# Kernel optimization log

Measured on AMD Instinct MI355X. Metric: run time of the kernel, lower is better.

Reference implementation:

```python
import jax, jax.numpy as jnp
import numpy as np

D_MODEL, N_HEADS, D_LLM = 1024, 16, 4096
D_KEYS = D_MODEL // N_HEADS  # 64


def setup_inputs() -> dict:
    key = jax.random.key(0)
    ks = jax.random.split(key, 11)
    s = lambda fan_in: 1.0 / np.sqrt(fan_in)
    inp = {
        "target_embedding": jax.random.normal(ks[0], (4, 2048, D_MODEL), jnp.float32),
        "source_embedding": jax.random.normal(ks[1], (4, 1024, D_LLM), jnp.float32),
        "value_embedding": jax.random.normal(ks[2], (4, 1024, D_LLM), jnp.float32),
        "Wq": jax.random.uniform(ks[3], (D_MODEL, D_KEYS * N_HEADS), jnp.float32, -s(D_MODEL), s(D_MODEL)),
        "bq": jax.random.uniform(ks[4], (D_KEYS * N_HEADS,), jnp.float32, -s(D_MODEL), s(D_MODEL)),
        "Wk": jax.random.uniform(ks[5], (D_LLM, D_KEYS * N_HEADS), jnp.float32, -s(D_LLM), s(D_LLM)),
        "bk": jax.random.uniform(ks[6], (D_KEYS * N_HEADS,), jnp.float32, -s(D_LLM), s(D_LLM)),
        "Wv": jax.random.uniform(ks[7], (D_LLM, D_KEYS * N_HEADS), jnp.float32, -s(D_LLM), s(D_LLM)),
        "bv": jax.random.uniform(ks[8], (D_KEYS * N_HEADS,), jnp.float32, -s(D_LLM), s(D_LLM)),
        "Wo": jax.random.uniform(ks[9], (D_KEYS * N_HEADS, D_MODEL), jnp.float32, -s(D_KEYS * N_HEADS), s(D_KEYS * N_HEADS)),
        "bo": jax.random.uniform(ks[10], (D_MODEL,), jnp.float32, -s(D_KEYS * N_HEADS), s(D_KEYS * N_HEADS)),
    }
    return inp


def reference(target_embedding, source_embedding, value_embedding,
              Wq, bq, Wk, bk, Wv, bv, Wo, bo):
    B, L, _ = target_embedding.shape
    _, S, _ = source_embedding.shape
    H, E = N_HEADS, D_KEYS
    q = (target_embedding @ Wq + bq).reshape(B, L, H, E)
    k = (source_embedding @ Wk + bk).reshape(B, S, H, E)
    v = (value_embedding @ Wv + bv).reshape(B, S, H, E)
    scale = 1.0 / np.sqrt(E)
    scores = jnp.einsum('blhe,bshe->bhls', q, k)  # [B,H,L,S]
    A = jax.nn.softmax(scale * scores, axis=-1)   # dropout = identity (eval mode)
    out = jnp.einsum('bhls,bshe->blhe', A, v).reshape(B, L, H * E)
    return out @ Wo + bo
```

## Files before the change

kernel.cpp:

```cpp
#include <hip/hip_runtime.h>
#include <hip/hip_bf16.h>

using bf16 = __hip_bfloat16;
typedef __attribute__((ext_vector_type(8))) short short8;
typedef __attribute__((ext_vector_type(4))) float f32x4;

static constexpr int Bc = 4, Lc = 2048, Sc = 1024;
static constexpr int DModel = 1024;

__device__ __forceinline__ void gload16(const void* g, void* l) {
  __builtin_amdgcn_global_load_lds((const __attribute__((address_space(1))) void*)g,
                                   (__attribute__((address_space(3))) void*)l,
                                   16, 0, 0);
}

__device__ __forceinline__ void wait_vm8()  { asm volatile("s_waitcnt vmcnt(8)" ::: "memory"); }
__device__ __forceinline__ void wait_vm6()  { asm volatile("s_waitcnt vmcnt(6)" ::: "memory"); }
__device__ __forceinline__ void wait_vm3()  { asm volatile("s_waitcnt vmcnt(3)" ::: "memory"); }
__device__ __forceinline__ void wait_vm2()  { asm volatile("s_waitcnt vmcnt(2)" ::: "memory"); }
__device__ __forceinline__ void wait_vm0()  { asm volatile("s_waitcnt vmcnt(0)" ::: "memory"); }
__device__ __forceinline__ void barrier_raw() { asm volatile("s_barrier" ::: "memory"); }

__global__ __launch_bounds__(256) void prep(
    const float* __restrict__ Wq, bf16* __restrict__ WqT,
    const float* __restrict__ Wk, bf16* __restrict__ WkT,
    const float* __restrict__ Wv, bf16* __restrict__ WvT,
    const float* __restrict__ Wo, bf16* __restrict__ WoT,
    const float* __restrict__ a, bf16* __restrict__ ao, long na4,
    const float* __restrict__ b, bf16* __restrict__ bo, long nb4,
    const float* __restrict__ c, bf16* __restrict__ co, long nc4) {
  __shared__ bf16 tile[32][33];
  int bid = blockIdx.x;
  if (bid < 10240) {
    const float* in; bf16* out; int R, l;
    if (bid < 1024)      { in = Wq; out = WqT; R = 1024; l = bid; }
    else if (bid < 5120) { in = Wk; out = WkT; R = 4096; l = bid - 1024; }
    else if (bid < 9216) { in = Wv; out = WvT; R = 4096; l = bid - 5120; }
    else                 { in = Wo; out = WoT; R = 1024; l = bid - 9216; }
    const int C = 1024;
    int bx = l & 31, by = l >> 5;
    int tx = threadIdx.x & 31, ty = threadIdx.x >> 5;
    int r0 = by * 32, c0 = bx * 32;
#pragma unroll
    for (int i = 0; i < 32; i += 8)
      tile[ty + i][tx] = __float2bfloat16(in[(long)(r0 + ty + i) * C + c0 + tx]);
    __syncthreads();
#pragma unroll
    for (int i = 0; i < 32; i += 8)
      out[(long)(c0 + ty + i) * R + r0 + tx] = tile[tx][ty + i];
  } else {
    int cb = bid - 10240;
    long total = na4 + nb4 + nc4;
    long stride = (long)(gridDim.x - 10240) * blockDim.x;
    for (long i = (long)cb * blockDim.x + threadIdx.x; i < total; i += stride) {
      const float* src; bf16* dst; long j;
      if (i < na4)            { src = a; dst = ao; j = i; }
      else if (i < na4 + nb4) { src = b; dst = bo; j = i - na4; }
      else                    { src = c; dst = co; j = i - na4 - nb4; }
      float4 v = reinterpret_cast<const float4*>(src)[j];
      alignas(8) bf16 t[4] = {__float2bfloat16(v.x), __float2bfloat16(v.y),
                              __float2bfloat16(v.z), __float2bfloat16(v.w)};
      reinterpret_cast<ushort4*>(dst)[j] = *reinterpret_cast<const ushort4*>(t);
    }
  }
}

__device__ __forceinline__ void gemm_bal_core(const bf16* __restrict__ A, const bf16* __restrict__ Bt,
                                              const float* __restrict__ bias,
                                              bf16* __restrict__ Cb, bf16* __restrict__ Cvt,
                                              int K, int bx, int by, bf16* lds) {
  const int tid = threadIdx.x;
  const int lane = tid & 63, g = lane >> 4, lm = lane & 15;
  const int wid = tid >> 6, wr = wid >> 1, wc = wid & 1;
  const long brow = (long)by * 256, bcol = (long)bx * 128;

  char* L = (char*)lds;
  const int rowA = tid >> 2;
  const int kg = (tid & 3) ^ ((rowA >> 1) & 3);
  const bf16* aS = A + (brow + rowA) * (long)K + kg * 8;
  const bf16* bS = Bt + (bcol + rowA) * (long)K + kg * 8;
  const long aOff1 = 128l * K;
  const int dA = tid * 16;

#define STAGEB(t_) {                                                     \
    const int _b = (t_) % 3; const long _ko = (long)(t_) * 32;           \
    gload16(aS + _ko,         L + _b * 24576 + dA);                      \
    gload16(aS + aOff1 + _ko, L + _b * 24576 + 8192 + dA);               \
    gload16(bS + _ko,         L + _b * 24576 + 16384 + dA); }

  f32x4 zero = {0.f, 0.f, 0.f, 0.f};
  f32x4 acc[4][4];
#pragma unroll
  for (int i = 0; i < 4; ++i)
#pragma unroll
    for (int j = 0; j < 4; ++j) acc[i][j] = zero;

  STAGEB(0);
  STAGEB(1);

  const int nt = K >> 5;
  for (int t = 0; t < nt; ++t) {
    if (t + 2 < nt)       { STAGEB(t + 2); wait_vm6(); }
    else if (t + 2 == nt) wait_vm3();
    else                  wait_vm0();
    barrier_raw();

    const char* Bf = L + (t % 3) * 24576;
    short8 aR[4], bR[4];
#pragma unroll
    for (int mi = 0; mi < 4; ++mi) {
      const int r = wr * 64 + mi * 16 + lm;
      aR[mi] = *reinterpret_cast<const short8*>(
          Bf + r * 64 + ((g ^ ((r >> 1) & 3)) << 4));
    }
#pragma unroll
    for (int ni = 0; ni < 4; ++ni) {
      const int r = wc * 64 + ni * 16 + lm;
      bR[ni] = *reinterpret_cast<const short8*>(
          Bf + 16384 + r * 64 + ((g ^ ((r >> 1) & 3)) << 4));
    }
    __builtin_amdgcn_s_setprio(1);
#pragma unroll
    for (int mi = 0; mi < 4; ++mi)
#pragma unroll
      for (int ni = 0; ni < 4; ++ni)
        acc[mi][ni] = __builtin_amdgcn_mfma_f32_16x16x32_bf16(aR[mi], bR[ni], acc[mi][ni], 0, 0, 0);
    __builtin_amdgcn_s_setprio(0);
    barrier_raw();
  }
#undef STAGEB

#pragma unroll
  for (int ni = 0; ni < 4; ++ni) {
    long n = bcol + wc * 64 + ni * 16 + lm;
    float bv = bias ? bias[n] : 0.f;
#pragma unroll
    for (int mi = 0; mi < 4; ++mi) {
      long m0 = brow + wr * 64 + mi * 16 + g * 4;
      if (Cvt) {
        long b = m0 >> 10, s0 = m0 & 1023;
        alignas(8) bf16 t4[4];
#pragma unroll
        for (int r = 0; r < 4; ++r) t4[r] = __float2bfloat16(acc[mi][ni][r] + bv);
        *reinterpret_cast<ushort4*>(Cvt + ((b << 10) + n) * 1024 + s0) =
            *reinterpret_cast<const ushort4*>(t4);
      } else {
#pragma unroll
        for (int r = 0; r < 4; ++r)
          Cb[(m0 + r) * 1024 + n] = __float2bfloat16(acc[mi][ni][r] + bv);
      }
    }
  }
}

__global__ __launch_bounds__(512, 4) void gemm_qkv_bal(
    const bf16* __restrict__ Ak, const bf16* __restrict__ Bk, const float* __restrict__ bk_, bf16* __restrict__ Ck, int Kk, int nbk,
    const bf16* __restrict__ Av, const bf16* __restrict__ Bv_, const float* __restrict__ bv_, bf16* __restrict__ CvT, int Kv, int nbv,
    const bf16* __restrict__ Aq, const bf16* __restrict__ Bq_, const float* __restrict__ bq_, bf16* __restrict__ Cq, int Kq) {
  __shared__ bf16 lds[36864];
  int bid = blockIdx.x;
  const bf16 *A, *Bt; const float* bias; bf16 *C = nullptr, *Cvt = nullptr; int K, l, nb;
  if (bid < nbk)            { A = Ak; Bt = Bk;  bias = bk_; C = Ck;    K = Kk; l = bid;             nb = nbk; }
  else if (bid < nbk + nbv) { A = Av; Bt = Bv_; bias = bv_; Cvt = CvT; K = Kv; l = bid - nbk;       nb = nbv; }
  else                      { A = Aq; Bt = Bq_; bias = bq_; C = Cq;   K = Kq; l = bid - nbk - nbv; nb = gridDim.x - nbk - nbv; }
  int g = (l & 7) * (nb >> 3) + (l >> 3);
  gemm_bal_core(A, Bt, bias, C, Cvt, K, g & 7, g >> 3, lds);
}

__device__ __forceinline__ void gemm_core(const bf16* __restrict__ A, const bf16* __restrict__ Bt,
                                          const float* __restrict__ bias,
                                          bf16* __restrict__ Cb, float* __restrict__ Cf,
                                          int N, int K, int bx, int by,
                                          bf16* As, bf16* Bs) {
  const int tid = threadIdx.x;
  const int lane = tid & 63, g = lane >> 4, lm = lane & 15;
  const int wid = tid >> 6, wr = wid >> 1, wc = wid & 1;
  const long brow = (long)by * 128, bcol = (long)bx * 128;

  const bf16* asrc[4];
  const bf16* bsrc[4];
  int dsto[4];
#pragma unroll
  for (int t = 0; t < 4; ++t) {
    int sl = tid + t * 256;
    int row = sl >> 3;
    int kg = (sl & 7) ^ (row & 7);
    asrc[t] = A + (brow + row) * (long)K + kg * 8;
    bsrc[t] = Bt + (bcol + row) * (long)K + kg * 8;
    dsto[t] = sl * 16;
  }

  f32x4 zero = {0.f, 0.f, 0.f, 0.f};
  f32x4 acc[4][4];
#pragma unroll
  for (int i = 0; i < 4; ++i)
#pragma unroll
    for (int j = 0; j < 4; ++j) acc[i][j] = zero;

  char* Asc = (char*)As;
  char* Bsc = (char*)Bs;

#pragma unroll
  for (int t = 0; t < 4; ++t) {
    gload16(asrc[t], Asc + dsto[t]);
    gload16(bsrc[t], Bsc + dsto[t]);
    asrc[t] += 64; bsrc[t] += 64;
  }

  const int nt = K >> 6;
  for (int i = 0; i < nt; ++i) {
    const int cur = i & 1;
    if (i + 1 < nt) {
      const int nxt = cur ^ 1;
#pragma unroll
      for (int t = 0; t < 4; ++t) {
        gload16(asrc[t], Asc + nxt * 16384 + dsto[t]);
        gload16(bsrc[t], Bsc + nxt * 16384 + dsto[t]);
        asrc[t] += 64; bsrc[t] += 64;
      }
      wait_vm8();
    } else {
      wait_vm0();
    }
    barrier_raw();

    const char* Ab = Asc + cur * 16384;
    const char* Bb = Bsc + cur * 16384;
    __builtin_amdgcn_s_setprio(1);
#pragma unroll
    for (int ks = 0; ks < 2; ++ks) {
      short8 af[4], bfv[4];
#pragma unroll
      for (int mi = 0; mi < 4; ++mi) {
        int m = wr * 64 + mi * 16 + lm;
        af[mi] = *reinterpret_cast<const short8*>(
            Ab + ((m * 128 + ks * 64 + g * 16) ^ ((m & 7) << 4)));
      }
#pragma unroll
      for (int ni = 0; ni < 4; ++ni) {
        int n = wc * 64 + ni * 16 + lm;
        bfv[ni] = *reinterpret_cast<const short8*>(
            Bb + ((n * 128 + ks * 64 + g * 16) ^ ((n & 7) << 4)));
      }
#pragma unroll
      for (int mi = 0; mi < 4; ++mi)
#pragma unroll
        for (int ni = 0; ni < 4; ++ni)
          acc[mi][ni] = __builtin_amdgcn_mfma_f32_16x16x32_bf16(af[mi], bfv[ni], acc[mi][ni], 0, 0, 0);
    }
    __builtin_amdgcn_s_setprio(0);
    barrier_raw();
  }

#pragma unroll
  for (int ni = 0; ni < 4; ++ni) {
    long n = bcol + wc * 64 + ni * 16 + lm;
    float bv = bias ? bias[n] : 0.f;
#pragma unroll
    for (int mi = 0; mi < 4; ++mi) {
      long m0 = brow + wr * 64 + mi * 16 + g * 4;
#pragma unroll
      for (int r = 0; r < 4; ++r) {
        float o = acc[mi][ni][r] + bv;
        if (Cb) Cb[(m0 + r) * N + n] = __float2bfloat16(o);
        else    Cf[(m0 + r) * N + n] = o;
      }
    }
  }
}

__global__ __launch_bounds__(256) void gemm_bt(const bf16* __restrict__ A,
                                               const bf16* __restrict__ Bt,
                                               const float* __restrict__ bias,
                                               bf16* __restrict__ Cb,
                                               float* __restrict__ Cf,
                                               int N, int K) {
  __shared__ bf16 As[2 * 128 * 64];
  __shared__ bf16 Bs[2 * 128 * 64];
  int bid = blockIdx.x;
  int g = (bid & 7) * (gridDim.x >> 3) + (bid >> 3);
  gemm_core(A, Bt, bias, Cb, Cf, N, K, g & 7, g >> 3, As, Bs);
}

__global__ __launch_bounds__(512) void attn_fused(const bf16* __restrict__ q,
                                                  const bf16* __restrict__ k,
                                                  const bf16* __restrict__ vT,
                                                  bf16* __restrict__ o) {
  constexpr float C2 = 0.18033688011112042f;
  constexpr float THR = 6.0f;
  __shared__ bf16 Kl[2][64 * 64];
  __shared__ bf16 Vl[2][64 * 64];
  __shared__ bf16 Pl[8][16 * 64];
  const int tid = threadIdx.x;
  const int lane = tid & 63, g = lane >> 4, lm = lane & 15;
  const int wid = tid >> 6;
  int bid = blockIdx.x;
  int gl = (bid & 7) * 128 + (bid >> 3);
  const int qt = gl & 15, bh = gl >> 4;
  const int b = bh >> 4, h = bh & 15;
  const int qbase = qt * 128 + wid * 16;

  const bf16* qrow = q + (long)(b * Lc + qbase + lm) * DModel + h * 64;
  short8 qa0 = *reinterpret_cast<const short8*>(qrow + g * 8);
  short8 qa1 = *reinterpret_cast<const short8*>(qrow + 32 + g * 8);
#pragma unroll
  for (int j = 0; j < 8; ++j) {
    union { ushort u; bf16 h; } cv;
    cv.u = (ushort)qa0[j];
    bf16 s0 = __float2bfloat16(__bfloat162float(cv.h) * C2);
    qa0[j] = (short)*reinterpret_cast<ushort*>(&s0);
    cv.u = (ushort)qa1[j];
    bf16 s1 = __float2bfloat16(__bfloat162float(cv.h) * C2);
    qa1[j] = (short)*reinterpret_cast<ushort*>(&s1);
  }

  const bf16* kbase = k + (long)b * Sc * DModel + h * 64;
  const bf16* vbase = vT + ((long)b * DModel + h * 64) * Sc;

  const int srow = tid >> 3;
  const int scg = (tid & 7) ^ (srow & 7);
  const bf16* ksrc = kbase + (long)srow * DModel + scg * 8;
  const bf16* vsrc = vbase + (long)srow * Sc + scg * 8;
  const int dsto = tid * 16;

  f32x4 zero = {0.f, 0.f, 0.f, 0.f};
  f32x4 accO[4];
#pragma unroll
  for (int i = 0; i < 4; ++i) accO[i] = zero;
  f32x4 accL = zero;
  float mst[4] = {-1e30f, -1e30f, -1e30f, -1e30f};

  short8 vones;
#pragma unroll
  for (int j = 0; j < 8; ++j) vones[j] = (short)0x3F80;

  char* Klc = (char*)Kl;
  char* Vlc = (char*)Vl;
  char* Plc = (char*)Pl + wid * (16 * 64 * 2);

  gload16(ksrc, Klc + dsto);
  gload16(vsrc, Vlc + dsto);
  ksrc += 64 * DModel; vsrc += 64;

  for (int j = 0; j < Sc / 64; ++j) {
    const int cur = j & 1;
    if (j + 1 < Sc / 64) {
      const int nxt = cur ^ 1;
      gload16(ksrc, Klc + nxt * 8192 + dsto);
      gload16(vsrc, Vlc + nxt * 8192 + dsto);
      ksrc += 64 * DModel; vsrc += 64;
      wait_vm2();
    } else {
      wait_vm0();
    }
    barrier_raw();

    const char* Kb = Klc + cur * 8192;
    const char* Vb = Vlc + cur * 8192;

    f32x4 scv[4];
    __builtin_amdgcn_s_setprio(1);
#pragma unroll
    for (int st = 0; st < 4; ++st) {
      int s = st * 16 + lm;
      int sw = (s & 7) << 4;
      short8 kb0 = *reinterpret_cast<const short8*>(Kb + ((s * 128 + g * 16) ^ sw));
      short8 kb1 = *reinterpret_cast<const short8*>(Kb + ((s * 128 + 64 + g * 16) ^ sw));
      f32x4 z = zero;
      z = __builtin_amdgcn_mfma_f32_16x16x32_bf16(qa0, kb0, z, 0, 0, 0);
      z = __builtin_amdgcn_mfma_f32_16x16x32_bf16(qa1, kb1, z, 0, 0, 0);
      scv[st] = z;
    }
    __builtin_amdgcn_s_setprio(0);

    float pmax[4];
#pragma unroll
    for (int r = 0; r < 4; ++r)
      pmax[r] = fmaxf(fmaxf(scv[0][r], scv[1][r]), fmaxf(scv[2][r], scv[3][r]));
    int need = 0;
#pragma unroll
    for (int r = 0; r < 4; ++r) need |= (pmax[r] > mst[r] + THR) ? 1 : 0;
    if (__any(need)) {
#pragma unroll
      for (int r = 0; r < 4; ++r) {
        float mx = pmax[r];
        mx = fmaxf(mx, __shfl_xor(mx, 1));
        mx = fmaxf(mx, __shfl_xor(mx, 2));
        mx = fmaxf(mx, __shfl_xor(mx, 4));
        mx = fmaxf(mx, __shfl_xor(mx, 8));
        float mnew = fmaxf(mst[r], mx);
        float corr = __builtin_amdgcn_exp2f(mst[r] - mnew);
        mst[r] = mnew;
        accL[r] *= corr;
#pragma unroll
        for (int et = 0; et < 4; ++et) accO[et][r] *= corr;
      }
    }
#pragma unroll
    for (int r = 0; r < 4; ++r) {
      int qq = g * 4 + r;
      int swp = (qq & 7) << 4;
#pragma unroll
      for (int st = 0; st < 4; ++st) {
        float p = __builtin_amdgcn_exp2f(scv[st][r] - mst[r]);
        *reinterpret_cast<bf16*>(Plc + ((qq * 128 + (st * 16 + lm) * 2) ^ swp)) =
            __float2bfloat16(p);
      }
    }

    __builtin_amdgcn_s_setprio(1);
#pragma unroll
    for (int sk = 0; sk < 2; ++sk) {
      short8 pa = *reinterpret_cast<const short8*>(
          Plc + ((lm * 128 + sk * 64 + g * 16) ^ ((lm & 7) << 4)));
      accL = __builtin_amdgcn_mfma_f32_16x16x32_bf16(pa, vones, accL, 0, 0, 0);
#pragma unroll
      for (int et = 0; et < 4; ++et) {
        int e = et * 16 + lm;
        short8 vb = *reinterpret_cast<const short8*>(
            Vb + ((e * 128 + sk * 64 + g * 16) ^ ((e & 7) << 4)));
        accO[et] = __builtin_amdgcn_mfma_f32_16x16x32_bf16(pa, vb, accO[et], 0, 0, 0);
      }
    }
    __builtin_amdgcn_s_setprio(0);
    barrier_raw();
  }

#pragma unroll
  for (int r = 0; r < 4; ++r) {
    float inv = 1.0f / accL[r];
    long row = (long)(b * Lc + qbase + g * 4 + r);
#pragma unroll
    for (int et = 0; et < 4; ++et)
      o[row * DModel + h * 64 + et * 16 + lm] = __float2bfloat16(accO[et][r] * inv);
  }
}

extern "C" void kernel_launch(void* const* d_in, const int* in_sizes, int n_in,
                              void* d_out, int out_size, void* d_ws, size_t ws_size,
                              hipStream_t stream) {
  const float* tgt = (const float*)d_in[0];
  const float* src = (const float*)d_in[1];
  const float* val = (const float*)d_in[2];
  const float* Wq  = (const float*)d_in[3];
  const float* bq  = (const float*)d_in[4];
  const float* Wk  = (const float*)d_in[5];
  const float* bk  = (const float*)d_in[6];
  const float* Wv  = (const float*)d_in[7];
  const float* bv  = (const float*)d_in[8];
  const float* Wo  = (const float*)d_in[9];
  const float* bo  = (const float*)d_in[10];
  float* out = (float*)d_out;
  char* ws = (char*)d_ws;

  const long n4_tgt = (long)8192 * 1024 / 4;
  const long n4_sv  = (long)4096 * 4096 / 4;

  if (ws_size < (132ul << 20)) return;

  bf16* WqT  = (bf16*)(ws + (0l   << 20));
  bf16* WkT  = (bf16*)(ws + (2l   << 20));
  bf16* WvT  = (bf16*)(ws + (10l  << 20));
  bf16* WoT  = (bf16*)(ws + (18l  << 20));
  bf16* tgtb = (bf16*)(ws + (20l  << 20));
  bf16* srcb = (bf16*)(ws + (36l  << 20));
  bf16* valb = (bf16*)(ws + (68l  << 20));
  bf16* qb   = (bf16*)(ws + (100l << 20));
  bf16* kb   = (bf16*)(ws + (116l << 20));
  bf16* vTb  = (bf16*)(ws + (124l << 20));
  bf16* attnb = tgtb;

  prep<<<10240 + 4096, 256, 0, stream>>>(Wq, WqT, Wk, WkT, Wv, WvT, Wo, WoT,
                                         tgt, tgtb, n4_tgt, src, srcb, n4_sv,
                                         val, valb, n4_sv);
  gemm_qkv_bal<<<512, 512, 0, stream>>>(srcb, WkT, bk, kb, 4096, 128,
                                        valb, WvT, bv, vTb, 4096, 128,
                                        tgtb, WqT, bq, qb, 1024);
  attn_fused<<<1024, 512, 0, stream>>>(qb, kb, vTb, attnb);
  gemm_bt<<<512, 256, 0, stream>>>(attnb, WoT, bo, (bf16*)nullptr, out, 1024, 1024);
}
```

Measured before the change: 227.9 us.

## Process two 16-row query groups per wave in attention to reuse K/V tiles

Each wave in the fused attention kernel now handles 32 query rows (two 16-row groups) instead of 16. Each workgroup covers 256 queries, so the grid drops from 1024 to 512 blocks. Every K/V tile loaded into LDS and every V fragment read from LDS now feeds twice as many MFMAs, which halves global K/V traffic and the per-query barrier and load overhead. In exchange each thread holds more registers (doubled accumulators and softmax state) and the P buffer in shared memory doubles. The smaller grid of 512 blocks may also underfill the GPU's compute units.

Measured after the change: 232.4 us. About the same (+1.9%).

```diff
diff --git a/kernel.cpp b/kernel.cpp
--- a/kernel.cpp
+++ b/kernel.cpp
@@ -282,36 +282,40 @@
   gemm_core(A, Bt, bias, Cb, Cf, N, K, g & 7, g >> 3, As, Bs);
 }
 
-__global__ __launch_bounds__(512) void attn_fused(const bf16* __restrict__ q,
-                                                  const bf16* __restrict__ k,
-                                                  const bf16* __restrict__ vT,
-                                                  bf16* __restrict__ o) {
+__global__ __launch_bounds__(512, 4) void attn_fused(const bf16* __restrict__ q,
+                                                     const bf16* __restrict__ k,
+                                                     const bf16* __restrict__ vT,
+                                                     bf16* __restrict__ o) {
   constexpr float C2 = 0.18033688011112042f;
   constexpr float THR = 6.0f;
   __shared__ bf16 Kl[2][64 * 64];
   __shared__ bf16 Vl[2][64 * 64];
-  __shared__ bf16 Pl[8][16 * 64];
+  __shared__ bf16 Pl[8][32 * 64];
   const int tid = threadIdx.x;
   const int lane = tid & 63, g = lane >> 4, lm = lane & 15;
   const int wid = tid >> 6;
   int bid = blockIdx.x;
-  int gl = (bid & 7) * 128 + (bid >> 3);
-  const int qt = gl & 15, bh = gl >> 4;
+  int gl = (bid & 7) * 64 + (bid >> 3);
+  const int qt = gl & 7, bh = gl >> 3;
   const int b = bh >> 4, h = bh & 15;
-  const int qbase = qt * 128 + wid * 16;
-
-  const bf16* qrow = q + (long)(b * Lc + qbase + lm) * DModel + h * 64;
-  short8 qa0 = *reinterpret_cast<const short8*>(qrow + g * 8);
-  short8 qa1 = *reinterpret_cast<const short8*>(qrow + 32 + g * 8);
-#pragma unroll
-  for (int j = 0; j < 8; ++j) {
-    union { ushort u; bf16 h; } cv;
-    cv.u = (ushort)qa0[j];
-    bf16 s0 = __float2bfloat16(__bfloat162float(cv.h) * C2);
-    qa0[j] = (short)*reinterpret_cast<ushort*>(&s0);
-    cv.u = (ushort)qa1[j];
-    bf16 s1 = __float2bfloat16(__bfloat162float(cv.h) * C2);
-    qa1[j] = (short)*reinterpret_cast<ushort*>(&s1);
+  const int qbase = qt * 256 + wid * 32;
+
+  short8 qa[2][2];
+#pragma unroll
+  for (int rg = 0; rg < 2; ++rg) {
+    const bf16* qrow = q + (long)(b * Lc + qbase + rg * 16 + lm) * DModel + h * 64;
+    qa[rg][0] = *reinterpret_cast<const short8*>(qrow + g * 8);
+    qa[rg][1] = *reinterpret_cast<const short8*>(qrow + 32 + g * 8);
+#pragma unroll
+    for (int j = 0; j < 8; ++j) {
+      union { ushort u; bf16 h; } cv;
+      cv.u = (ushort)qa[rg][0][j];
+      bf16 s0 = __float2bfloat16(__bfloat162float(cv.h) * C2);
+      qa[rg][0][j] = (short)*reinterpret_cast<ushort*>(&s0);
+      cv.u = (ushort)qa[rg][1][j];
+      bf16 s1 = __float2bfloat16(__bfloat162float(cv.h) * C2);
+      qa[rg][1][j] = (short)*reinterpret_cast<ushort*>(&s1);
+    }
   }
 
   const bf16* kbase = k + (long)b * Sc * DModel + h * 64;
@@ -324,11 +328,14 @@
   const int dsto = tid * 16;
 
   f32x4 zero = {0.f, 0.f, 0.f, 0.f};
-  f32x4 accO[4];
-#pragma unroll
-  for (int i = 0; i < 4; ++i) accO[i] = zero;
-  f32x4 accL = zero;
-  float mst[4] = {-1e30f, -1e30f, -1e30f, -1e30f};
+  f32x4 accO[2][4];
+#pragma unroll
+  for (int rg = 0; rg < 2; ++rg)
+#pragma unroll
+    for (int i = 0; i < 4; ++i) accO[rg][i] = zero;
+  f32x4 accL[2] = {zero, zero};
+  float mst[2][4] = {{-1e30f, -1e30f, -1e30f, -1e30f},
+                     {-1e30f, -1e30f, -1e30f, -1e30f}};
 
   short8 vones;
 #pragma unroll
@@ -336,7 +343,7 @@
 
   char* Klc = (char*)Kl;
   char* Vlc = (char*)Vl;
-  char* Plc = (char*)Pl + wid * (16 * 64 * 2);
+  char* Plc = (char*)Pl + wid * (32 * 64 * 2);
 
   gload16(ksrc, Klc + dsto);
   gload16(vsrc, Vlc + dsto);
@@ -358,68 +365,78 @@
     const char* Kb = Klc + cur * 8192;
     const char* Vb = Vlc + cur * 8192;
 
-    f32x4 scv[4];
+#pragma unroll
+    for (int rg = 0; rg < 2; ++rg) {
+      f32x4 scv[4];
+      __builtin_amdgcn_s_setprio(1);
+#pragma unroll
+      for (int st = 0; st < 4; ++st) {
+        int s = st * 16 + lm;
+        int sw = (s & 7) << 4;
+        short8 kb0 = *reinterpret_cast<const short8*>(Kb + ((s * 128 + g * 16) ^ sw));
+        short8 kb1 = *reinterpret_cast<const short8*>(Kb + ((s * 128 + 64 + g * 16) ^ sw));
+        f32x4 z = zero;
+        z = __builtin_amdgcn_mfma_f32_16x16x32_bf16(qa[rg][0], kb0, z, 0, 0, 0);
+        z = __builtin_amdgcn_mfma_f32_16x16x32_bf16(qa[rg][1], kb1, z, 0, 0, 0);
+        scv[st] = z;
+      }
+      __builtin_amdgcn_s_setprio(0);
+
+      float pmax[4];
+#pragma unroll
+      for (int r = 0; r < 4; ++r)
+        pmax[r] = fmaxf(fmaxf(scv[0][r], scv[1][r]), fmaxf(scv[2][r], scv[3][r]));
+      int need = 0;
+#pragma unroll
+      for (int r = 0; r < 4; ++r) need |= (pmax[r] > mst[rg][r] + THR) ? 1 : 0;
+      if (__any(need)) {
+#pragma unroll
+        for (int r = 0; r < 4; ++r) {
+          float mx = pmax[r];
+          mx = fmaxf(mx, __shfl_xor(mx, 1));
+          mx = fmaxf(mx, __shfl_xor(mx, 2));
+          mx = fmaxf(mx, __shfl_xor(mx, 4));
+          mx = fmaxf(mx, __shfl_xor(mx, 8));
+          float mnew = fmaxf(mst[rg][r], mx);
+          float corr = __builtin_amdgcn_exp2f(mst[rg][r] - mnew);
+          mst[rg][r] = mnew;
+          accL[rg][r] *= corr;
+#pragma unroll
+          for (int et = 0; et < 4; ++et) accO[rg][et][r] *= corr;
+        }
+      }
+#pragma unroll
+      for (int r = 0; r < 4; ++r) {
+        int pq = rg * 16 + g * 4 + r;
+        int swp = (pq & 7) << 4;
+#pragma unroll
+        for (int st = 0; st < 4; ++st) {
+          float p = __builtin_amdgcn_exp2f(scv[st][r] - mst[rg][r]);
+          *reinterpret_cast<bf16*>(Plc + ((pq * 128 + (st * 16 + lm) * 2) ^ swp)) =
+              __float2bfloat16(p);
+        }
+      }
+    }
+
     __builtin_amdgcn_s_setprio(1);
 #pragma unroll
-    for (int st = 0; st < 4; ++st) {
-      int s = st * 16 + lm;
-      int sw = (s & 7) << 4;
-      short8 kb0 = *reinterpret_cast<const short8*>(Kb + ((s * 128 + g * 16) ^ sw));
-      short8 kb1 = *reinterpret_cast<const short8*>(Kb + ((s * 128 + 64 + g * 16) ^ sw));
-      f32x4 z = zero;
-      z = __builtin_amdgcn_mfma_f32_16x16x32_bf16(qa0, kb0, z, 0, 0, 0);
-      z = __builtin_amdgcn_mfma_f32_16x16x32_bf16(qa1, kb1, z, 0, 0, 0);
-      scv[st] = z;
-    }
-    __builtin_amdgcn_s_setprio(0);
-
-    float pmax[4];
-#pragma unroll
-    for (int r = 0; r < 4; ++r)
-      pmax[r] = fmaxf(fmaxf(scv[0][r], scv[1][r]), fmaxf(scv[2][r], scv[3][r]));
-    int need = 0;
-#pragma unroll
-    for (int r = 0; r < 4; ++r) need |= (pmax[r] > mst[r] + THR) ? 1 : 0;
-    if (__any(need)) {
-#pragma unroll
-      for (int r = 0; r < 4; ++r) {
-        float mx = pmax[r];
-        mx = fmaxf(mx, __shfl_xor(mx, 1));
-        mx = fmaxf(mx, __shfl_xor(mx, 2));
-        mx = fmaxf(mx, __shfl_xor(mx, 4));
-        mx = fmaxf(mx, __shfl_xor(mx, 8));
-        float mnew = fmaxf(mst[r], mx);
-        float corr = __builtin_amdgcn_exp2f(mst[r] - mnew);
-        mst[r] = mnew;
-        accL[r] *= corr;
-#pragma unroll
-        for (int et = 0; et < 4; ++et) accO[et][r] *= corr;
-      }
-    }
-#pragma unroll
-    for (int r = 0; r < 4; ++r) {
-      int qq = g * 4 + r;
-      int swp = (qq & 7) << 4;
-#pragma unroll
-      for (int st = 0; st < 4; ++st) {
-        float p = __builtin_amdgcn_exp2f(scv[st][r] - mst[r]);
-        *reinterpret_cast<bf16*>(Plc + ((qq * 128 + (st * 16 + lm) * 2) ^ swp)) =
-            __float2bfloat16(p);
-      }
-    }
-
-    __builtin_amdgcn_s_setprio(1);
-#pragma unroll
     for (int sk = 0; sk < 2; ++sk) {
-      short8 pa = *reinterpret_cast<const short8*>(
-          Plc + ((lm * 128 + sk * 64 + g * 16) ^ ((lm & 7) << 4)));
-      accL = __builtin_amdgcn_mfma_f32_16x16x32_bf16(pa, vones, accL, 0, 0, 0);
+      short8 pa[2];
+#pragma unroll
+      for (int rg = 0; rg < 2; ++rg) {
+        int pr = rg * 16 + lm;
+        pa[rg] = *reinterpret_cast<const short8*>(
+            Plc + ((pr * 128 + sk * 64 + g * 16) ^ ((pr & 7) << 4)));
+      }
+      accL[0] = __builtin_amdgcn_mfma_f32_16x16x32_bf16(pa[0], vones, accL[0], 0, 0, 0);
+      accL[1] = __builtin_amdgcn_mfma_f32_16x16x32_bf16(pa[1], vones, accL[1], 0, 0, 0);
 #pragma unroll
       for (int et = 0; et < 4; ++et) {
         int e = et * 16 + lm;
         short8 vb = *reinterpret_cast<const short8*>(
             Vb + ((e * 128 + sk * 64 + g * 16) ^ ((e & 7) << 4)));
-        accO[et] = __builtin_amdgcn_mfma_f32_16x16x32_bf16(pa, vb, accO[et], 0, 0, 0);
+        accO[0][et] = __builtin_amdgcn_mfma_f32_16x16x32_bf16(pa[0], vb, accO[0][et], 0, 0, 0);
+        accO[1][et] = __builtin_amdgcn_mfma_f32_16x16x32_bf16(pa[1], vb, accO[1][et], 0, 0, 0);
       }
     }
     __builtin_amdgcn_s_setprio(0);
@@ -427,13 +444,15 @@
   }
 
 #pragma unroll
-  for (int r = 0; r < 4; ++r) {
-    float inv = 1.0f / accL[r];
-    long row = (long)(b * Lc + qbase + g * 4 + r);
-#pragma unroll
-    for (int et = 0; et < 4; ++et)
-      o[row * DModel + h * 64 + et * 16 + lm] = __float2bfloat16(accO[et][r] * inv);
-  }
+  for (int rg = 0; rg < 2; ++rg)
+#pragma unroll
+    for (int r = 0; r < 4; ++r) {
+      float inv = 1.0f / accL[rg][r];
+      long row = (long)(b * Lc + qbase + rg * 16 + g * 4 + r);
+#pragma unroll
+      for (int et = 0; et < 4; ++et)
+        o[row * DModel + h * 64 + et * 16 + lm] = __float2bfloat16(accO[rg][et][r] * inv);
+    }
 }
 
 extern "C" void kernel_launch(void* const* d_in, const int* in_sizes, int n_in,
@@ -476,6 +495,6 @@
   gemm_qkv_bal<<<512, 512, 0, stream>>>(srcb, WkT, bk, kb, 4096, 128,
                                         valb, WvT, bv, vTb, 4096, 128,
                                         tgtb, WqT, bq, qb, 1024);
-  attn_fused<<<1024, 512, 0, stream>>>(qb, kb, vTb, attnb);
+  attn_fused<<<512, 512, 0, stream>>>(qb, kb, vTb, attnb);
   gemm_bt<<<512, 256, 0, stream>>>(attnb, WoT, bo, (bf16*)nullptr, out, 1024, 1024);
 }
```
